# Kernel tuning notes

Measured on AMD Instinct MI355X. Metric: run time of the kernel, lower is better.

## Reference

```python
import jax, jax.numpy as jnp
import numpy as np

B, T, H, S, C = 16, 1024, 1024, 32, 3
NH, DH = 16, 64  # heads, head_dim (NH*DH == H)
GAMMA = 2.0      # focal gamma
EPS = 1e-7       # deberta layer_norm_eps


def setup_inputs() -> dict:
    key = jax.random.key(0)
    ks = jax.random.split(key, 32)
    Hh = H // 2

    def n(k, shape, scale=0.02):
        return jax.random.normal(k, shape, jnp.float32) * scale

    chunk = T // S  # contiguous non-overlapping spans
    heads = jnp.tile(jnp.arange(S, dtype=jnp.int32) * chunk, (B, 1))
    tails = heads + chunk
    inp = {
        'hidden_states': jax.random.normal(ks[0], (B, T, H), jnp.float32),
        'span_head_idxs': heads,
        'span_tail_idxs': tails,
        'span_attention_mask': jnp.ones((B, S), jnp.int32),
        'labels': jax.random.randint(ks[1], (B, S), 0, C, jnp.int32),
        'weights_factor': jax.random.uniform(ks[2], (B, S), jnp.float32) + 0.5,
        # BiLSTM params (torch gate order i,f,g,o)
        'lstm_Wih_f': n(ks[3], (4 * Hh, H)), 'lstm_Whh_f': n(ks[4], (4 * Hh, Hh)), 'lstm_b_f': jnp.zeros((4 * Hh,), jnp.float32),
        'lstm_Wih_b': n(ks[5], (4 * Hh, H)), 'lstm_Whh_b': n(ks[6], (4 * Hh, Hh)), 'lstm_b_b': jnp.zeros((4 * Hh,), jnp.float32),
        # LayerNorm after span pooling
        'ln1_g': jnp.ones((H,), jnp.float32), 'ln1_b': jnp.zeros((H,), jnp.float32),
        # span attention (DebertaV2Attention, relative_attention=False => vanilla MHA)
        'Wq': n(ks[7], (H, H)), 'bq': jnp.zeros((H,), jnp.float32),
        'Wk': n(ks[8], (H, H)), 'bk': jnp.zeros((H,), jnp.float32),
        'Wv': n(ks[9], (H, H)), 'bv': jnp.zeros((H,), jnp.float32),
        'Wo': n(ks[10], (H, H)), 'bo': jnp.zeros((H,), jnp.float32),
        'ln2_g': jnp.ones((H,), jnp.float32), 'ln2_b': jnp.zeros((H,), jnp.float32),
        # classifier
        'Wc': n(ks[11], (H, C)), 'bc': jnp.zeros((C,), jnp.float32),
    }
    return inp


def _layernorm(x, g, b, eps=EPS):
    m = jnp.mean(x, -1, keepdims=True)
    v = jnp.var(x, -1, keepdims=True)
    return (x - m) * jax.lax.rsqrt(v + eps) * g + b


def _lstm_dir(x, Wih, Whh, b, reverse):
    # x: [B,T,H] -> hs [B,T,Hh]
    Hh = Whh.shape[1]
    xs = jnp.einsum('bti,gi->btg', x, Wih) + b  # precompute input projections
    if reverse:
        xs = xs[:, ::-1]

    def step(carry, xt):
        h, c = carry
        g = xt + h @ Whh.T
        i, f, gg, o = jnp.split(g, 4, axis=-1)
        c = jax.nn.sigmoid(f) * c + jax.nn.sigmoid(i) * jnp.tanh(gg)
        h = jax.nn.sigmoid(o) * jnp.tanh(c)
        return (h, c), h

    h0 = jnp.zeros((x.shape[0], Hh), x.dtype)
    _, hs = jax.lax.scan(step, (h0, h0), jnp.swapaxes(xs, 0, 1))
    hs = jnp.swapaxes(hs, 0, 1)
    if reverse:
        hs = hs[:, ::-1]
    return hs


def _forward(hidden_states, span_head_idxs, span_tail_idxs, span_attention_mask,
             labels, weights_factor,
             lstm_Wih_f, lstm_Whh_f, lstm_b_f, lstm_Wih_b, lstm_Whh_b, lstm_b_b,
             ln1_g, ln1_b, Wq, bq, Wk, bk, Wv, bv, Wo, bo, ln2_g, ln2_b, Wc, bc):
    # BiLSTM over tokens
    enc = jnp.concatenate([
        _lstm_dir(hidden_states, lstm_Wih_f, lstm_Whh_f, lstm_b_f, False),
        _lstm_dir(hidden_states, lstm_Wih_b, lstm_Whh_b, lstm_b_b, True),
    ], axis=-1)  # [B,T,H]

    # fused span mean-pooling: mean over tokens p with head < p < tail
    pos = jnp.arange(T)
    smask = (pos[None, None, :] > span_head_idxs[:, :, None]) & \
            (pos[None, None, :] < span_tail_idxs[:, :, None])  # [B,S,T]
    smf = smask.astype(enc.dtype)
    counts = jnp.maximum(smf.sum(-1, keepdims=True), 1.0)
    feat = jnp.einsum('bst,bth->bsh', smf, enc) / counts  # [B,S,H]
    feat = _layernorm(feat, ln1_g, ln1_b)

    # span self-attention (standard MHA + residual LayerNorm)
    def split_heads(x):
        return x.reshape(B, S, NH, DH)
    q = split_heads(feat @ Wq + bq)
    k = split_heads(feat @ Wk + bk)
    v = split_heads(feat @ Wv + bv)
    scores = jnp.einsum('bqhd,bkhd->bhqk', q, k) / np.sqrt(DH).astype(np.float32)
    am = span_attention_mask.astype(jnp.bool_)
    m2 = am[:, None, None, :] & am[:, None, :, None]  # [B,1,S,S]
    scores = jnp.where(m2, scores, jnp.float32(-1e9))
    attn = jax.nn.softmax(scores, axis=-1)
    ctx = jnp.einsum('bhqk,bkhd->bqhd', attn, v).reshape(B, S, H)
    feat2 = _layernorm(ctx @ Wo + bo + feat, ln2_g, ln2_b)

    # classifier (dropouts are identity at eval; the 5-way average collapses)
    logits = feat2 @ Wc + bc  # [B,S,C]

    # losses
    logp = jax.nn.log_softmax(logits, axis=-1)
    lab = labels
    valid = (lab >= 0)
    lp_t = jnp.take_along_axis(logp, jnp.clip(lab, 0)[..., None], axis=-1)[..., 0]
    spanm = span_attention_mask.astype(jnp.float32) * valid.astype(jnp.float32)
    ce = -lp_t * weights_factor
    ce_loss = jnp.sum(ce * spanm) / jnp.maximum(jnp.sum(spanm), 1.0)
    pt = jnp.exp(logp)
    mod = (1.0 - pt) ** GAMMA * logp
    ft = -jnp.take_along_axis(mod, jnp.clip(lab, 0)[..., None], axis=-1)[..., 0]
    vm = valid.astype(jnp.float32)
    focal_loss = jnp.sum(ft * vm) / jnp.maximum(jnp.sum(vm), 1.0)
    return ce_loss + focal_loss


def reference(hidden_states, span_head_idxs, span_tail_idxs, span_attention_mask,
              labels, weights_factor,
              lstm_Wih_f, lstm_Whh_f, lstm_b_f, lstm_Wih_b, lstm_Whh_b, lstm_b_b,
              ln1_g, ln1_b, Wq, bq, Wk, bk, Wv, bv, Wo, bo, ln2_g, ln2_b, Wc, bc):
    return _forward(hidden_states, span_head_idxs, span_tail_idxs, span_attention_mask,
                    labels, weights_factor,
                    lstm_Wih_f, lstm_Whh_f, lstm_b_f, lstm_Wih_b, lstm_Whh_b, lstm_b_b,
                    ln1_g, ln1_b, Wq, bq, Wk, bk, Wv, bv, Wo, bo, ln2_g, ln2_b, Wc, bc)
```

## Files before the change

### kernel.cpp

```cpp
#include <hip/hip_runtime.h>
#include <stdint.h>

typedef __attribute__((ext_vector_type(4))) float    f32x4;
typedef __attribute__((ext_vector_type(8))) short    s16x8;
typedef __attribute__((ext_vector_type(4))) uint32_t u32x4;
typedef __attribute__((ext_vector_type(4))) uint16_t u16x4;
typedef __attribute__((ext_vector_type(8))) uint16_t u16x8;

#define SENT 0xFFFFFFFFu

__device__ __forceinline__ uint16_t f2bf(float f) {
    uint32_t u = __float_as_uint(f);
    u = u + 0x7FFFu + ((u >> 16) & 1u);
    return (uint16_t)(u >> 16);
}
__device__ __forceinline__ float bf2f(uint16_t h) {
    return __uint_as_float(((uint32_t)h) << 16);
}
__device__ __forceinline__ float sigm(float x) {
    return __builtin_amdgcn_rcpf(1.0f + __expf(-x));
}
__device__ __forceinline__ float tanh_f(float x) {
    float e = __expf(2.0f * x);
    return 1.0f - 2.0f * __builtin_amdgcn_rcpf(e + 1.0f);
}

__global__ void kinit(uint32_t* __restrict__ hx) {
    size_t i = ((size_t)blockIdx.x * 256 + threadIdx.x) * 4;
    *(u32x4*)(hx + i) = u32x4{SENT, SENT, SENT, SENT};
}

__global__ void kprep(const float* __restrict__ wihf, const float* __restrict__ wihb,
                      const float* __restrict__ whhf, const float* __restrict__ whhb,
                      const float* __restrict__ bq, const float* __restrict__ bk,
                      const float* __restrict__ bv,
                      uint16_t* __restrict__ wihbf, uint16_t* __restrict__ whhbf,
                      float* __restrict__ biasqkv) {
    size_t i = (size_t)blockIdx.x * 256 + threadIdx.x;
    if (i < 2097152) {
        wihbf[i] = f2bf(wihf[i]);
    } else if (i < 4194304) {
        wihbf[i] = f2bf(wihb[i - 2097152]);
    } else if (i < 5242880) {
        whhbf[i - 4194304] = f2bf(whhf[i - 4194304]);
    } else if (i < 6291456) {
        whhbf[i - 4194304] = f2bf(whhb[i - 5242880]);
    } else if (i < 6294528) {
        size_t k = i - 6291456;
        biasqkv[k] = (k < 1024) ? bq[k] : (k < 2048) ? bk[k - 1024] : bv[k - 2048];
    }
}

__global__ void ktrans(const float* __restrict__ Wq, const float* __restrict__ Wk,
                       const float* __restrict__ Wv, const float* __restrict__ Wo,
                       uint16_t* __restrict__ out) {
    const float* W = (blockIdx.z == 0) ? Wq : (blockIdx.z == 1) ? Wk : (blockIdx.z == 2) ? Wv : Wo;
    __shared__ float t[32][33];
    int x  = blockIdx.x * 32 + threadIdx.x;
    int y0 = blockIdx.y * 32 + threadIdx.y;
#pragma unroll
    for (int i = 0; i < 4; i++)
        t[threadIdx.y + 8 * i][threadIdx.x] = W[(size_t)(y0 + 8 * i) * 1024 + x];
    __syncthreads();
    int ox  = blockIdx.y * 32 + threadIdx.x;
    int oy0 = blockIdx.x * 32 + threadIdx.y;
#pragma unroll
    for (int i = 0; i < 4; i++)
        out[((size_t)blockIdx.z * 1024 + oy0 + 8 * i) * 1024 + ox] = f2bf(t[threadIdx.x][threadIdx.y + 8 * i]);
}

template <int AF32>
__global__ __launch_bounds__(256) void gemm_k(const void* __restrict__ Av,
                                              const uint16_t* __restrict__ B,
                                              const float* __restrict__ bias,
                                              uint16_t* __restrict__ C, int M, int N) {
    __shared__ uint16_t lA[128 * 40];
    __shared__ uint16_t lB[128 * 40];
    const int tid = threadIdx.x;
    const int m0 = blockIdx.y * 128, n0 = blockIdx.x * 128;
    const int srow = tid >> 1, skh = (tid & 1) * 16;
    const int lane = tid & 63, wid = tid >> 6;
    const int wm = wid >> 1, wn = wid & 1;
    const int fn = lane & 15, fq = lane >> 4;
    f32x4 acc[4][4];
#pragma unroll
    for (int a = 0; a < 4; a++)
#pragma unroll
        for (int b = 0; b < 4; b++) acc[a][b] = f32x4{0.f, 0.f, 0.f, 0.f};

    for (int kt = 0; kt < 32; kt++) {
        if (AF32) {
            const float* A = (const float*)Av + (size_t)(m0 + srow) * 1024 + kt * 32 + skh;
#pragma unroll
            for (int i = 0; i < 4; i++) {
                f32x4 t = *(const f32x4*)(A + i * 4);
                u16x4 p;
                p[0] = f2bf(t[0]); p[1] = f2bf(t[1]); p[2] = f2bf(t[2]); p[3] = f2bf(t[3]);
                *(u16x4*)&lA[srow * 40 + skh + i * 4] = p;
            }
        } else {
            const uint16_t* A = (const uint16_t*)Av + (size_t)(m0 + srow) * 1024 + kt * 32 + skh;
            *(u16x8*)&lA[srow * 40 + skh]     = *(const u16x8*)(A);
            *(u16x8*)&lA[srow * 40 + skh + 8] = *(const u16x8*)(A + 8);
        }
        const uint16_t* Bp = B + (size_t)(n0 + srow) * 1024 + kt * 32 + skh;
        *(u16x8*)&lB[srow * 40 + skh]     = *(const u16x8*)(Bp);
        *(u16x8*)&lB[srow * 40 + skh + 8] = *(const u16x8*)(Bp + 8);
        __syncthreads();
        s16x8 af[4], bfv[4];
#pragma unroll
        for (int mt = 0; mt < 4; mt++) af[mt] = *(const s16x8*)&lA[(wm * 64 + mt * 16 + fn) * 40 + fq * 8];
#pragma unroll
        for (int nt = 0; nt < 4; nt++) bfv[nt] = *(const s16x8*)&lB[(wn * 64 + nt * 16 + fn) * 40 + fq * 8];
#pragma unroll
        for (int mt = 0; mt < 4; mt++)
#pragma unroll
            for (int nt = 0; nt < 4; nt++)
                acc[mt][nt] = __builtin_amdgcn_mfma_f32_16x16x32_bf16(af[mt], bfv[nt], acc[mt][nt], 0, 0, 0);
        __syncthreads();
    }
#pragma unroll
    for (int nt = 0; nt < 4; nt++) {
        int col = n0 + wn * 64 + nt * 16 + fn;
        float bvv = bias ? bias[col] : 0.0f;
#pragma unroll
        for (int mt = 0; mt < 4; mt++) {
            int row0 = m0 + wm * 64 + mt * 16 + fq * 4;
#pragma unroll
            for (int i = 0; i < 4; i++)
                C[(size_t)(row0 + i) * N + col] = f2bf(acc[mt][nt][i] + bvv);
        }
    }
}

__global__ __launch_bounds__(256, 1) void krecur(const uint16_t* __restrict__ whhbf,
                                                 const uint16_t* __restrict__ xs,
                                                 uint32_t* __restrict__ hx) {
    const int wg = blockIdx.x;
    const int dir = wg >> 3, g = wg & 7;
    const int tid = threadIdx.x;
    const int w = tid >> 6, lane = tid & 63;
    const int j = g * 4 + w;
    const int n = lane & 15, q = lane >> 4;

    __shared__ uint16_t lh[2][8192];

    s16x8 Bf[4][16];
    {
        const uint16_t* wb = whhbf + (size_t)dir * 2048 * 512;
#pragma unroll
        for (int t4 = 0; t4 < 4; t4++)
#pragma unroll
            for (int s = 0; s < 16; s++)
                Bf[t4][s] = *(const s16x8*)(wb + (size_t)(t4 * 512 + j * 16 + n) * 512 + s * 32 + q * 8);
    }
    float c[4] = {0.f, 0.f, 0.f, 0.f};
    const uint16_t* xsp = xs + (size_t)dir * 16384 * 2048;
    uint32_t* hxp = hx + (size_t)dir * 1024 * 4096;

    uint16_t xv[4][4];
    {
        const int pf = dir ? 1023 : 0;
#pragma unroll
        for (int t4 = 0; t4 < 4; t4++)
#pragma unroll
            for (int i = 0; i < 4; i++)
                xv[t4][i] = xsp[((size_t)(4 * q + i) * 1024 + pf) * 2048 + t4 * 512 + j * 16 + n];
    }

    for (int t = 0; t < 1024; t++) {
        const int p = dir ? (1023 - t) : t;
        const int buf = t & 1;

        f32x4 acc[4];
#pragma unroll
        for (int t4 = 0; t4 < 4; t4++) acc[t4] = f32x4{0.f, 0.f, 0.f, 0.f};

        if (t > 0) {
            const int pp = dir ? (p + 1) : (p - 1);
            const uint32_t* hbase = hxp + ((size_t)pp * 16 + n) * 256 + q * 4;
            u32x4 Ah[4];
            for (;;) {
#pragma unroll
                for (int si = 0; si < 4; si++) {
                    const uint32_t* ap = hbase + (w * 4 + si) * 16;
                    asm volatile("global_load_dwordx4 %0, %1, off sc1"
                                 : "=v"(Ah[si]) : "v"(ap) : "memory");
                }
                asm volatile("s_waitcnt vmcnt(0)" ::: "memory");
                uint32_t mx = 0;
#pragma unroll
                for (int si = 0; si < 4; si++)
#pragma unroll
                    for (int wd = 0; wd < 4; wd++) mx = (Ah[si][wd] > mx) ? Ah[si][wd] : mx;
                if (__ballot(mx == SENT) == 0ull) break;
            }
#pragma unroll
            for (int si = 0; si < 4; si++) {
                int s = w * 4 + si;
                *(u32x4*)&lh[buf][s * 512 + q * 128 + n * 8] = Ah[si];
            }
            __syncthreads();
#pragma unroll
            for (int s = 0; s < 16; s++) {
                s16x8 Af = *(const s16x8*)&lh[buf][s * 512 + q * 128 + n * 8];
#pragma unroll
                for (int t4 = 0; t4 < 4; t4++)
                    acc[t4] = __builtin_amdgcn_mfma_f32_16x16x32_bf16(Af, Bf[t4][s], acc[t4], 0, 0, 0);
            }
        }

        uint16_t xn[4][4];
        if (t < 1023) {
            const int pn = dir ? (p - 1) : (p + 1);
#pragma unroll
            for (int t4 = 0; t4 < 4; t4++)
#pragma unroll
                for (int i = 0; i < 4; i++)
                    xn[t4][i] = xsp[((size_t)(4 * q + i) * 1024 + pn) * 2048 + t4 * 512 + j * 16 + n];
        }

        float g4[4][4];
#pragma unroll
        for (int t4 = 0; t4 < 4; t4++)
#pragma unroll
            for (int i = 0; i < 4; i++)
                g4[t4][i] = acc[t4][i] + bf2f(xv[t4][i]);

#pragma unroll
        for (int i = 0; i < 4; i++) {
            float ig = sigm(g4[0][i]);
            float fg = sigm(g4[1][i]);
            float gg = tanh_f(g4[2][i]);
            float og = sigm(g4[3][i]);
            c[i] = fg * c[i] + ig * gg;
            float hv = og * tanh_f(c[i]);
            uint32_t mine = (uint32_t)f2bf(hv);
            uint32_t part = __shfl_xor(mine, 1);
            if ((n & 1) == 0) {
                uint32_t pack = mine | (part << 16);
                __hip_atomic_store(hxp + ((size_t)p * 16 + 4 * q + i) * 256 + j * 8 + (n >> 1),
                                   pack, __ATOMIC_RELAXED, __HIP_MEMORY_SCOPE_AGENT);
            }
        }

        if (t < 1023) {
#pragma unroll
            for (int t4 = 0; t4 < 4; t4++)
#pragma unroll
                for (int i = 0; i < 4; i++) xv[t4][i] = xn[t4][i];
        }
    }
}

__global__ __launch_bounds__(256) void kpool(const uint32_t* __restrict__ hx,
                                             const int* __restrict__ heads,
                                             const int* __restrict__ tails,
                                             const float* __restrict__ g,
                                             const float* __restrict__ bb,
                                             float* __restrict__ feat,
                                             uint16_t* __restrict__ featb) {
    const int m = blockIdx.x;
    const int b = m >> 5;
    const int tid = threadIdx.x;
    const int h0 = tid * 4;
    const int dir = h0 >> 9, hid = h0 & 511;
    int p0 = heads[m] + 1; if (p0 < 0) p0 = 0;
    int p1 = tails[m];     if (p1 > 1024) p1 = 1024;
    float a0 = 0, a1 = 0, a2 = 0, a3 = 0;
    int cnt = p1 - p0; if (cnt < 1) cnt = 1;
    for (int p = p0; p < p1; p++) {
        const uint32_t* e = hx + (((size_t)dir * 1024 + p) * 16 + b) * 256 + (hid >> 1);
        uint32_t w0 = e[0], w1 = e[1];
        a0 += bf2f((uint16_t)(w0 & 0xffff)); a1 += bf2f((uint16_t)(w0 >> 16));
        a2 += bf2f((uint16_t)(w1 & 0xffff)); a3 += bf2f((uint16_t)(w1 >> 16));
    }
    float inv = 1.0f / (float)cnt;
    float x0 = a0 * inv, x1 = a1 * inv, x2 = a2 * inv, x3 = a3 * inv;
    float ls = x0 + x1 + x2 + x3;
    float lq = x0 * x0 + x1 * x1 + x2 * x2 + x3 * x3;
#pragma unroll
    for (int o = 32; o > 0; o >>= 1) { ls += __shfl_down(ls, o); lq += __shfl_down(lq, o); }
    __shared__ float rs_[4], rq_[4], st_[2];
    const int lane = tid & 63, wid = tid >> 6;
    if (lane == 0) { rs_[wid] = ls; rq_[wid] = lq; }
    __syncthreads();
    if (tid == 0) {
        float S = rs_[0] + rs_[1] + rs_[2] + rs_[3];
        float Q = rq_[0] + rq_[1] + rq_[2] + rq_[3];
        float mean = S * (1.0f / 1024.0f);
        float var = Q * (1.0f / 1024.0f) - mean * mean;
        st_[0] = mean;
        st_[1] = rsqrtf(var + 1e-7f);
    }
    __syncthreads();
    float mean = st_[0], rstd = st_[1];
    size_t ob = (size_t)m * 1024 + h0;
    float y0 = (x0 - mean) * rstd * g[h0 + 0] + bb[h0 + 0];
    float y1 = (x1 - mean) * rstd * g[h0 + 1] + bb[h0 + 1];
    float y2 = (x2 - mean) * rstd * g[h0 + 2] + bb[h0 + 2];
    float y3 = (x3 - mean) * rstd * g[h0 + 3] + bb[h0 + 3];
    feat[ob + 0] = y0; feat[ob + 1] = y1; feat[ob + 2] = y2; feat[ob + 3] = y3;
    featb[ob + 0] = f2bf(y0); featb[ob + 1] = f2bf(y1);
    featb[ob + 2] = f2bf(y2); featb[ob + 3] = f2bf(y3);
}

__global__ __launch_bounds__(64) void kattn(const uint16_t* __restrict__ qkv,
                                            const int* __restrict__ am,
                                            uint16_t* __restrict__ ctxb) {
    const int bb_ = blockIdx.x >> 4, nh = blockIdx.x & 15;
    const int lane = threadIdx.x;
    __shared__ float qs[32][65], ks[32][65], vs[32][65];
    __shared__ float ps[32][33];
    for (int s = 0; s < 32; s++) {
        const uint16_t* base = qkv + (size_t)(bb_ * 32 + s) * 3072 + nh * 64;
        qs[s][lane] = bf2f(base[lane]);
        ks[s][lane] = bf2f(base[1024 + lane]);
        vs[s][lane] = bf2f(base[2048 + lane]);
    }
    __syncthreads();
    const int r = lane >> 1, ch = (lane & 1) * 16;
    const int amr = am[bb_ * 32 + r];
    float sc[16];
#pragma unroll
    for (int c0 = 0; c0 < 16; c0++) {
        int cc = ch + c0;
        float a = 0;
        for (int d = 0; d < 64; d++) a += qs[r][d] * ks[cc][d];
        a *= 0.125f;
        if (!(amr && am[bb_ * 32 + cc])) a = -1e9f;
        sc[c0] = a;
    }
    float mx = sc[0];
#pragma unroll
    for (int c0 = 1; c0 < 16; c0++) mx = fmaxf(mx, sc[c0]);
    mx = fmaxf(mx, __shfl_xor(mx, 1));
    float se = 0;
#pragma unroll
    for (int c0 = 0; c0 < 16; c0++) { sc[c0] = __expf(sc[c0] - mx); se += sc[c0]; }
    se += __shfl_xor(se, 1);
    float inv = __builtin_amdgcn_rcpf(se);
#pragma unroll
    for (int c0 = 0; c0 < 16; c0++) ps[r][ch + c0] = sc[c0] * inv;
    __syncthreads();
    for (int r2 = 0; r2 < 32; r2++) {
        float a = 0;
        for (int cc = 0; cc < 32; cc++) a += ps[r2][cc] * vs[cc][lane];
        ctxb[(size_t)(bb_ * 32 + r2) * 1024 + nh * 64 + lane] = f2bf(a);
    }
}

__global__ __launch_bounds__(256) void kln2(const uint16_t* __restrict__ oproj,
                                            const float* __restrict__ feat,
                                            const float* __restrict__ g,
                                            const float* __restrict__ bb,
                                            float* __restrict__ feat2) {
    const int m = blockIdx.x, tid = threadIdx.x;
    const int h0 = tid * 4;
    size_t base = (size_t)m * 1024 + h0;
    u16x4 ov = *(const u16x4*)(oproj + base);
    float x0 = bf2f(ov[0]) + feat[base + 0];
    float x1 = bf2f(ov[1]) + feat[base + 1];
    float x2 = bf2f(ov[2]) + feat[base + 2];
    float x3 = bf2f(ov[3]) + feat[base + 3];
    float ls = x0 + x1 + x2 + x3;
    float lq = x0 * x0 + x1 * x1 + x2 * x2 + x3 * x3;
#pragma unroll
    for (int o = 32; o > 0; o >>= 1) { ls += __shfl_down(ls, o); lq += __shfl_down(lq, o); }
    __shared__ float rs_[4], rq_[4], st_[2];
    const int lane = tid & 63, wid = tid >> 6;
    if (lane == 0) { rs_[wid] = ls; rq_[wid] = lq; }
    __syncthreads();
    if (tid == 0) {
        float S = rs_[0] + rs_[1] + rs_[2] + rs_[3];
        float Q = rq_[0] + rq_[1] + rq_[2] + rq_[3];
        float mean = S * (1.0f / 1024.0f);
        float var = Q * (1.0f / 1024.0f) - mean * mean;
        st_[0] = mean;
        st_[1] = rsqrtf(var + 1e-7f);
    }
    __syncthreads();
    float mean = st_[0], rstd = st_[1];
    feat2[base + 0] = (x0 - mean) * rstd * g[h0 + 0] + bb[h0 + 0];
    feat2[base + 1] = (x1 - mean) * rstd * g[h0 + 1] + bb[h0 + 1];
    feat2[base + 2] = (x2 - mean) * rstd * g[h0 + 2] + bb[h0 + 2];
    feat2[base + 3] = (x3 - mean) * rstd * g[h0 + 3] + bb[h0 + 3];
}

__global__ __launch_bounds__(64) void kloss(const float* __restrict__ feat2,
                                            const float* __restrict__ Wc,
                                            const float* __restrict__ bc,
                                            const int* __restrict__ labels,
                                            const int* __restrict__ am,
                                            const float* __restrict__ wf,
                                            float* __restrict__ accum) {
    const int m = blockIdx.x, lane = threadIdx.x;
    float l0 = 0, l1 = 0, l2 = 0;
    for (int k = lane; k < 1024; k += 64) {
        float f = feat2[(size_t)m * 1024 + k];
        l0 += f * Wc[k * 3 + 0];
        l1 += f * Wc[k * 3 + 1];
        l2 += f * Wc[k * 3 + 2];
    }
#pragma unroll
    for (int o = 32; o > 0; o >>= 1) {
        l0 += __shfl_down(l0, o);
        l1 += __shfl_down(l1, o);
        l2 += __shfl_down(l2, o);
    }
    if (lane == 0) {
        l0 += bc[0]; l1 += bc[1]; l2 += bc[2];
        float mx = fmaxf(l0, fmaxf(l1, l2));
        float e0 = __expf(l0 - mx), e1 = __expf(l1 - mx), e2 = __expf(l2 - mx);
        float lse = mx + __logf(e0 + e1 + e2);
        float lp[3] = {l0 - lse, l1 - lse, l2 - lse};
        int lab = labels[m];
        float validf = (lab >= 0) ? 1.0f : 0.0f;
        int labc = lab < 0 ? 0 : lab;
        float amv = (am[m] != 0) ? 1.0f : 0.0f;
        float spanm = amv * validf;
        float ce = -lp[labc] * wf[m];
        float pt = __expf(lp[labc]);
        float om = 1.0f - pt;
        float ft = -(om * om * lp[labc]);
        atomicAdd(accum + 0, ce * spanm);
        atomicAdd(accum + 1, spanm);
        atomicAdd(accum + 2, ft * validf);
        atomicAdd(accum + 3, validf);
    }
}

__global__ void kfinal(const float* __restrict__ accum, float* __restrict__ out) {
    out[0] = accum[0] / fmaxf(accum[1], 1.0f) + accum[2] / fmaxf(accum[3], 1.0f);
}

extern "C" void kernel_launch(void* const* d_in, const int* in_sizes, int n_in,
                              void* d_out, int out_size, void* d_ws, size_t ws_size,
                              hipStream_t stream) {
    const float* hs   = (const float*)d_in[0];
    const int* heads  = (const int*)d_in[1];
    const int* tails  = (const int*)d_in[2];
    const int* amask  = (const int*)d_in[3];
    const int* labels = (const int*)d_in[4];
    const float* wfac = (const float*)d_in[5];
    const float* wihf = (const float*)d_in[6];
    const float* whhf = (const float*)d_in[7];
    const float* lbf  = (const float*)d_in[8];
    const float* wihb = (const float*)d_in[9];
    const float* whhb = (const float*)d_in[10];
    const float* lbb  = (const float*)d_in[11];
    const float* ln1g = (const float*)d_in[12];
    const float* ln1b = (const float*)d_in[13];
    const float* Wq   = (const float*)d_in[14];
    const float* bq   = (const float*)d_in[15];
    const float* Wk   = (const float*)d_in[16];
    const float* bk   = (const float*)d_in[17];
    const float* Wv   = (const float*)d_in[18];
    const float* bv   = (const float*)d_in[19];
    const float* Wo   = (const float*)d_in[20];
    const float* bo   = (const float*)d_in[21];
    const float* ln2g = (const float*)d_in[22];
    const float* ln2b = (const float*)d_in[23];
    const float* Wc   = (const float*)d_in[24];
    const float* bc   = (const float*)d_in[25];

    char* ws = (char*)d_ws;
    float* accum    = (float*)(ws + 1024);
    uint16_t* whhbf = (uint16_t*)(ws + 4096);
    uint16_t* wihbf = (uint16_t*)(ws + 4198400);
    uint16_t* wqkvo = (uint16_t*)(ws + 12587008);
    float* biasqkv  = (float*)(ws + 20975616);
    uint16_t* xs    = (uint16_t*)(ws + 20987904);
    uint32_t* hx    = (uint32_t*)(ws + 155205632);
    float* feat     = (float*)(ws + 188760064);
    uint16_t* featb = (uint16_t*)(ws + 190857216);
    uint16_t* qkvb  = (uint16_t*)(ws + 191905792);
    uint16_t* ctxb  = (uint16_t*)(ws + 195051520);
    uint16_t* oprojb= (uint16_t*)(ws + 196100096);
    float* feat2    = (float*)(ws + 197148672);

    hipMemsetAsync(ws, 0, 4096, stream);

    kinit<<<8192, 256, 0, stream>>>(hx);

    kprep<<<24588, 256, 0, stream>>>(wihf, wihb, whhf, whhb, bq, bk, bv, wihbf, whhbf, biasqkv);
    ktrans<<<dim3(32, 32, 4), dim3(32, 8), 0, stream>>>(Wq, Wk, Wv, Wo, wqkvo);

    gemm_k<1><<<dim3(16, 128), 256, 0, stream>>>(hs, wihbf, lbf, xs, 16384, 2048);
    gemm_k<1><<<dim3(16, 128), 256, 0, stream>>>(hs, wihbf + (size_t)2048 * 1024, lbb,
                                                 xs + (size_t)16384 * 2048, 16384, 2048);

    krecur<<<16, 256, 0, stream>>>(whhbf, xs, hx);

    kpool<<<512, 256, 0, stream>>>(hx, heads, tails, ln1g, ln1b, feat, featb);

    gemm_k<0><<<dim3(24, 4), 256, 0, stream>>>(featb, wqkvo, biasqkv, qkvb, 512, 3072);

    kattn<<<256, 64, 0, stream>>>(qkvb, amask, ctxb);

    gemm_k<0><<<dim3(8, 4), 256, 0, stream>>>(ctxb, wqkvo + (size_t)3072 * 1024, bo, oprojb, 512, 1024);

    kln2<<<512, 256, 0, stream>>>(oprojb, feat, ln2g, ln2b, feat2);
    kloss<<<512, 64, 0, stream>>>(feat2, Wc, bc, labels, amask, wfac, accum);
    kfinal<<<1, 1, 0, stream>>>(accum, (float*)d_out);
}
```

Before: 4.195 ms.

## Fuse LSTM input-projection GEMM with recurrence via sentinel-flagged streaming

```diff
diff --git a/kernel.cpp b/kernel.cpp
--- a/kernel.cpp
+++ b/kernel.cpp
@@ -25,9 +25,9 @@
     return 1.0f - 2.0f * __builtin_amdgcn_rcpf(e + 1.0f);
 }
 
-__global__ void kinit(uint32_t* __restrict__ hx) {
+__global__ void kinit(uint32_t* __restrict__ base) {
     size_t i = ((size_t)blockIdx.x * 256 + threadIdx.x) * 4;
-    *(u32x4*)(hx + i) = u32x4{SENT, SENT, SENT, SENT};
+    *(u32x4*)(base + i) = u32x4{SENT, SENT, SENT, SENT};
 }
 
 __global__ void kprep(const float* __restrict__ wihf, const float* __restrict__ wihb,
@@ -69,8 +69,7 @@
         out[((size_t)blockIdx.z * 1024 + oy0 + 8 * i) * 1024 + ox] = f2bf(t[threadIdx.x][threadIdx.y + 8 * i]);
 }
 
-template <int AF32>
-__global__ __launch_bounds__(256) void gemm_k(const void* __restrict__ Av,
+__global__ __launch_bounds__(256) void gemm_k(const uint16_t* __restrict__ A0,
                                               const uint16_t* __restrict__ B,
                                               const float* __restrict__ bias,
                                               uint16_t* __restrict__ C, int M, int N) {
@@ -89,20 +88,9 @@
         for (int b = 0; b < 4; b++) acc[a][b] = f32x4{0.f, 0.f, 0.f, 0.f};
 
     for (int kt = 0; kt < 32; kt++) {
-        if (AF32) {
-            const float* A = (const float*)Av + (size_t)(m0 + srow) * 1024 + kt * 32 + skh;
-#pragma unroll
-            for (int i = 0; i < 4; i++) {
-                f32x4 t = *(const f32x4*)(A + i * 4);
-                u16x4 p;
-                p[0] = f2bf(t[0]); p[1] = f2bf(t[1]); p[2] = f2bf(t[2]); p[3] = f2bf(t[3]);
-                *(u16x4*)&lA[srow * 40 + skh + i * 4] = p;
-            }
-        } else {
-            const uint16_t* A = (const uint16_t*)Av + (size_t)(m0 + srow) * 1024 + kt * 32 + skh;
-            *(u16x8*)&lA[srow * 40 + skh]     = *(const u16x8*)(A);
-            *(u16x8*)&lA[srow * 40 + skh + 8] = *(const u16x8*)(A + 8);
-        }
+        const uint16_t* A = A0 + (size_t)(m0 + srow) * 1024 + kt * 32 + skh;
+        *(u16x8*)&lA[srow * 40 + skh]     = *(const u16x8*)(A);
+        *(u16x8*)&lA[srow * 40 + skh + 8] = *(const u16x8*)(A + 8);
         const uint16_t* Bp = B + (size_t)(n0 + srow) * 1024 + kt * 32 + skh;
         *(u16x8*)&lB[srow * 40 + skh]     = *(const u16x8*)(Bp);
         *(u16x8*)&lB[srow * 40 + skh + 8] = *(const u16x8*)(Bp + 8);
@@ -133,122 +121,240 @@
     }
 }
 
-__global__ __launch_bounds__(256, 1) void krecur(const uint16_t* __restrict__ whhbf,
-                                                 const uint16_t* __restrict__ xs,
+__global__ __launch_bounds__(256, 1) void kfused(const uint16_t* __restrict__ whhbf,
+                                                 const uint16_t* __restrict__ wihbf,
+                                                 const float* __restrict__ hs,
+                                                 const float* __restrict__ lbf,
+                                                 const float* __restrict__ lbb,
+                                                 uint16_t* __restrict__ xs,
                                                  uint32_t* __restrict__ hx) {
-    const int wg = blockIdx.x;
-    const int dir = wg >> 3, g = wg & 7;
-    const int tid = threadIdx.x;
-    const int w = tid >> 6, lane = tid & 63;
-    const int j = g * 4 + w;
-    const int n = lane & 15, q = lane >> 4;
-
-    __shared__ uint16_t lh[2][8192];
-
-    s16x8 Bf[4][16];
-    {
-        const uint16_t* wb = whhbf + (size_t)dir * 2048 * 512;
-#pragma unroll
-        for (int t4 = 0; t4 < 4; t4++)
-#pragma unroll
-            for (int s = 0; s < 16; s++)
-                Bf[t4][s] = *(const s16x8*)(wb + (size_t)(t4 * 512 + j * 16 + n) * 512 + s * 32 + q * 8);
-    }
-    float c[4] = {0.f, 0.f, 0.f, 0.f};
-    const uint16_t* xsp = xs + (size_t)dir * 16384 * 2048;
-    uint32_t* hxp = hx + (size_t)dir * 1024 * 4096;
-
-    uint16_t xv[4][4];
-    {
-        const int pf = dir ? 1023 : 0;
-#pragma unroll
-        for (int t4 = 0; t4 < 4; t4++)
-#pragma unroll
-            for (int i = 0; i < 4; i++)
-                xv[t4][i] = xsp[((size_t)(4 * q + i) * 1024 + pf) * 2048 + t4 * 512 + j * 16 + n];
-    }
-
-    for (int t = 0; t < 1024; t++) {
-        const int p = dir ? (1023 - t) : t;
-        const int buf = t & 1;
-
-        f32x4 acc[4];
-#pragma unroll
-        for (int t4 = 0; t4 < 4; t4++) acc[t4] = f32x4{0.f, 0.f, 0.f, 0.f};
-
-        if (t > 0) {
-            const int pp = dir ? (p + 1) : (p - 1);
-            const uint32_t* hbase = hxp + ((size_t)pp * 16 + n) * 256 + q * 4;
+    __shared__ uint16_t smem[16384];
+
+    if (blockIdx.x < 16) {
+        const int wg = blockIdx.x;
+        const int dir = wg >> 3, g = wg & 7;
+        const int tid = threadIdx.x;
+        const int w = tid >> 6, lane = tid & 63;
+        const int j = g * 4 + w;
+        const int n = lane & 15, q = lane >> 4;
+
+        s16x8 Bf[4][16];
+        {
+            const uint16_t* wb = whhbf + (size_t)dir * 2048 * 512;
+#pragma unroll
+            for (int t4 = 0; t4 < 4; t4++)
+#pragma unroll
+                for (int s = 0; s < 16; s++)
+                    Bf[t4][s] = *(const s16x8*)(wb + (size_t)(t4 * 512 + j * 16 + n) * 512 + s * 32 + q * 8);
+        }
+        float c[4] = {0.f, 0.f, 0.f, 0.f};
+        const uint32_t* xsp32 = (const uint32_t*)(xs + (size_t)dir * 16384 * 2048);
+        uint32_t* hxp = hx + (size_t)dir * 1024 * 4096;
+
+        uint32_t xvA[4][4], xvB[4][4];
+        {
+            const int pf = dir ? 1023 : 0;
+#pragma unroll
+            for (int t4 = 0; t4 < 4; t4++)
+#pragma unroll
+                for (int i = 0; i < 4; i++) {
+                    const uint32_t* ap = xsp32 + ((size_t)(4 * q + i) * 1024 + pf) * 1024
+                                       + ((t4 * 512 + j * 16 + n) >> 1);
+                    asm volatile("global_load_dword %0, %1, off sc1"
+                                 : "=v"(xvA[t4][i]) : "v"(ap) : "memory");
+                }
+        }
+
+        auto rstep = [&](int t, uint32_t (&xc)[4][4], uint32_t (&xn)[4][4]) {
+            const int p = dir ? (1023 - t) : t;
+            const int buf = t & 1;
             u32x4 Ah[4];
-            for (;;) {
+            const uint32_t* hbase = nullptr;
+            if (t > 0) {
+                const int pp = dir ? (p + 1) : (p - 1);
+                hbase = hxp + ((size_t)pp * 16 + n) * 256 + q * 4;
 #pragma unroll
                 for (int si = 0; si < 4; si++) {
                     const uint32_t* ap = hbase + (w * 4 + si) * 16;
                     asm volatile("global_load_dwordx4 %0, %1, off sc1"
                                  : "=v"(Ah[si]) : "v"(ap) : "memory");
                 }
+            }
+            if (t < 1023) {
+                const int pn = dir ? (p - 1) : (p + 1);
+#pragma unroll
+                for (int t4 = 0; t4 < 4; t4++)
+#pragma unroll
+                    for (int i = 0; i < 4; i++) {
+                        const uint32_t* ap = xsp32 + ((size_t)(4 * q + i) * 1024 + pn) * 1024
+                                           + ((t4 * 512 + j * 16 + n) >> 1);
+                        asm volatile("global_load_dword %0, %1, off sc1"
+                                     : "=v"(xn[t4][i]) : "v"(ap) : "memory");
+                    }
+                asm volatile("s_waitcnt vmcnt(16)" ::: "memory");
+            } else {
                 asm volatile("s_waitcnt vmcnt(0)" ::: "memory");
-                uint32_t mx = 0;
-#pragma unroll
-                for (int si = 0; si < 4; si++)
-#pragma unroll
-                    for (int wd = 0; wd < 4; wd++) mx = (Ah[si][wd] > mx) ? Ah[si][wd] : mx;
-                if (__ballot(mx == SENT) == 0ull) break;
             }
-#pragma unroll
-            for (int si = 0; si < 4; si++) {
-                int s = w * 4 + si;
-                *(u32x4*)&lh[buf][s * 512 + q * 128 + n * 8] = Ah[si];
+
+            f32x4 acc[4];
+#pragma unroll
+            for (int t4 = 0; t4 < 4; t4++) acc[t4] = f32x4{0.f, 0.f, 0.f, 0.f};
+
+            if (t > 0) {
+                for (;;) {
+                    uint32_t bad = 0;
+#pragma unroll
+                    for (int si = 0; si < 4; si++)
+#pragma unroll
+                        for (int wd = 0; wd < 4; wd++)
+                            if (Ah[si][wd] == SENT) bad = 1;
+                    if (__ballot(bad) == 0ull) break;
+#pragma unroll
+                    for (int si = 0; si < 4; si++) {
+                        const uint32_t* ap = hbase + (w * 4 + si) * 16;
+                        asm volatile("global_load_dwordx4 %0, %1, off sc1"
+                                     : "=v"(Ah[si]) : "v"(ap) : "memory");
+                    }
+                    asm volatile("s_waitcnt vmcnt(0)" ::: "memory");
+                }
+#pragma unroll
+                for (int si = 0; si < 4; si++) {
+                    int s = w * 4 + si;
+                    *(u32x4*)&smem[buf * 8192 + s * 512 + q * 128 + n * 8] = Ah[si];
+                }
+                __syncthreads();
+#pragma unroll
+                for (int s = 0; s < 16; s++) {
+                    s16x8 Af = *(const s16x8*)&smem[buf * 8192 + s * 512 + q * 128 + n * 8];
+#pragma unroll
+                    for (int t4 = 0; t4 < 4; t4++)
+                        acc[t4] = __builtin_amdgcn_mfma_f32_16x16x32_bf16(Af, Bf[t4][s], acc[t4], 0, 0, 0);
+                }
             }
+
+            for (;;) {
+                uint32_t bad = 0;
+#pragma unroll
+                for (int t4 = 0; t4 < 4; t4++)
+#pragma unroll
+                    for (int i = 0; i < 4; i++)
+                        if (xc[t4][i] == SENT) bad = 1;
+                if (__ballot(bad) == 0ull) break;
+#pragma unroll
+                for (int t4 = 0; t4 < 4; t4++)
+#pragma unroll
+                    for (int i = 0; i < 4; i++) {
+                        const uint32_t* ap = xsp32 + ((size_t)(4 * q + i) * 1024 + p) * 1024
+                                           + ((t4 * 512 + j * 16 + n) >> 1);
+                        asm volatile("global_load_dword %0, %1, off sc1"
+                                     : "=v"(xc[t4][i]) : "v"(ap) : "memory");
+                    }
+                asm volatile("s_waitcnt vmcnt(0)" ::: "memory");
+            }
+
+            float g4[4][4];
+#pragma unroll
+            for (int t4 = 0; t4 < 4; t4++)
+#pragma unroll
+                for (int i = 0; i < 4; i++) {
+                    uint32_t pr = xc[t4][i];
+                    uint16_t xv16 = (n & 1) ? (uint16_t)(pr >> 16) : (uint16_t)(pr & 0xffff);
+                    g4[t4][i] = acc[t4][i] + bf2f(xv16);
+                }
+#pragma unroll
+            for (int i = 0; i < 4; i++) {
+                float ig = sigm(g4[0][i]);
+                float fg = sigm(g4[1][i]);
+                float gg = tanh_f(g4[2][i]);
+                float og = sigm(g4[3][i]);
+                c[i] = fg * c[i] + ig * gg;
+                float hv = og * tanh_f(c[i]);
+                uint32_t mine = (uint32_t)f2bf(hv);
+                uint32_t part = __shfl_xor(mine, 1);
+                if ((n & 1) == 0) {
+                    uint32_t pack = mine | (part << 16);
+                    __hip_atomic_store(hxp + ((size_t)p * 16 + 4 * q + i) * 256 + j * 8 + (n >> 1),
+                                       pack, __ATOMIC_RELAXED, __HIP_MEMORY_SCOPE_AGENT);
+                }
+            }
+        };
+
+        for (int t2 = 0; t2 < 1024; t2 += 2) {
+            rstep(t2,     xvA, xvB);
+            rstep(t2 + 1, xvB, xvA);
+        }
+    } else {
+        const int gb = blockIdx.x - 16;
+        const int dirg = gb & 1;
+        const int k = gb >> 1;
+        const int prorder = k >> 8;
+        const int rem = k & 255;
+        const int bidx = rem >> 4;
+        const int ntile = rem & 15;
+        const int prange = dirg ? (7 - prorder) : prorder;
+        const size_t mbase = (size_t)bidx * 1024 + (size_t)prange * 128;
+        const int n0 = ntile * 128;
+        const uint16_t* Bw = wihbf + (size_t)dirg * 2048 * 1024;
+        const float* biasg = dirg ? lbb : lbf;
+        uint16_t* Cx = xs + (size_t)dirg * 16384 * 2048;
+
+        uint16_t* lA = smem;
+        uint16_t* lB = smem + 5120;
+        const int tid = threadIdx.x;
+        const int srow = tid >> 1, skh = (tid & 1) * 16;
+        const int lane = tid & 63, wid = tid >> 6;
+        const int wm = wid >> 1, wn = wid & 1;
+        const int fn = lane & 15, fq = lane >> 4;
+        f32x4 acc[4][4];
+#pragma unroll
+        for (int a = 0; a < 4; a++)
+#pragma unroll
+            for (int b = 0; b < 4; b++) acc[a][b] = f32x4{0.f, 0.f, 0.f, 0.f};
+
+        for (int kt = 0; kt < 32; kt++) {
+            const float* A = hs + (mbase + srow) * 1024 + kt * 32 + skh;
+#pragma unroll
+            for (int i = 0; i < 4; i++) {
+                f32x4 tv = *(const f32x4*)(A + i * 4);
+                u16x4 pk;
+                pk[0] = f2bf(tv[0]); pk[1] = f2bf(tv[1]); pk[2] = f2bf(tv[2]); pk[3] = f2bf(tv[3]);
+                *(u16x4*)&lA[srow * 40 + skh + i * 4] = pk;
+            }
+            const uint16_t* Bp = Bw + (size_t)(n0 + srow) * 1024 + kt * 32 + skh;
+            *(u16x8*)&lB[srow * 40 + skh]     = *(const u16x8*)(Bp);
+            *(u16x8*)&lB[srow * 40 + skh + 8] = *(const u16x8*)(Bp + 8);
             __syncthreads();
-#pragma unroll
-            for (int s = 0; s < 16; s++) {
-                s16x8 Af = *(const s16x8*)&lh[buf][s * 512 + q * 128 + n * 8];
-#pragma unroll
-                for (int t4 = 0; t4 < 4; t4++)
-                    acc[t4] = __builtin_amdgcn_mfma_f32_16x16x32_bf16(Af, Bf[t4][s], acc[t4], 0, 0, 0);
+            s16x8 af[4], bfv[4];
+#pragma unroll
+            for (int mt = 0; mt < 4; mt++) af[mt] = *(const s16x8*)&lA[(wm * 64 + mt * 16 + fn) * 40 + fq * 8];
+#pragma unroll
+            for (int nt = 0; nt < 4; nt++) bfv[nt] = *(const s16x8*)&lB[(wn * 64 + nt * 16 + fn) * 40 + fq * 8];
+#pragma unroll
+            for (int mt = 0; mt < 4; mt++)
+#pragma unroll
+                for (int nt = 0; nt < 4; nt++)
+                    acc[mt][nt] = __builtin_amdgcn_mfma_f32_16x16x32_bf16(af[mt], bfv[nt], acc[mt][nt], 0, 0, 0);
+            __syncthreads();
+        }
+#pragma unroll
+        for (int nt = 0; nt < 4; nt++) {
+            int col = n0 + wn * 64 + nt * 16 + fn;
+            float bvv = biasg[col];
+#pragma unroll
+            for (int mt = 0; mt < 4; mt++) {
+                int rowoff = wm * 64 + mt * 16 + fq * 4;
+#pragma unroll
+                for (int i = 0; i < 4; i++) {
+                    uint32_t mine = (uint32_t)f2bf(acc[mt][nt][i] + bvv);
+                    uint32_t part = __shfl_xor(mine, 1);
+                    if ((fn & 1) == 0) {
+                        uint32_t pack = mine | (part << 16);
+                        size_t grow = mbase + rowoff + i;
+                        __hip_atomic_store((uint32_t*)(Cx + grow * 2048 + col), pack,
+                                           __ATOMIC_RELAXED, __HIP_MEMORY_SCOPE_AGENT);
+                    }
+                }
             }
-        }
-
-        uint16_t xn[4][4];
-        if (t < 1023) {
-            const int pn = dir ? (p - 1) : (p + 1);
-#pragma unroll
-            for (int t4 = 0; t4 < 4; t4++)
-#pragma unroll
-                for (int i = 0; i < 4; i++)
-                    xn[t4][i] = xsp[((size_t)(4 * q + i) * 1024 + pn) * 2048 + t4 * 512 + j * 16 + n];
-        }
-
-        float g4[4][4];
-#pragma unroll
-        for (int t4 = 0; t4 < 4; t4++)
-#pragma unroll
-            for (int i = 0; i < 4; i++)
-                g4[t4][i] = acc[t4][i] + bf2f(xv[t4][i]);
-
-#pragma unroll
-        for (int i = 0; i < 4; i++) {
-            float ig = sigm(g4[0][i]);
-            float fg = sigm(g4[1][i]);
-            float gg = tanh_f(g4[2][i]);
-            float og = sigm(g4[3][i]);
-            c[i] = fg * c[i] + ig * gg;
-            float hv = og * tanh_f(c[i]);
-            uint32_t mine = (uint32_t)f2bf(hv);
-            uint32_t part = __shfl_xor(mine, 1);
-            if ((n & 1) == 0) {
-                uint32_t pack = mine | (part << 16);
-                __hip_atomic_store(hxp + ((size_t)p * 16 + 4 * q + i) * 256 + j * 8 + (n >> 1),
-                                   pack, __ATOMIC_RELAXED, __HIP_MEMORY_SCOPE_AGENT);
-            }
-        }
-
-        if (t < 1023) {
-#pragma unroll
-            for (int t4 = 0; t4 < 4; t4++)
-#pragma unroll
-                for (int i = 0; i < 4; i++) xv[t4][i] = xn[t4][i];
         }
     }
 }
@@ -481,24 +587,20 @@
 
     hipMemsetAsync(ws, 0, 4096, stream);
 
-    kinit<<<8192, 256, 0, stream>>>(hx);
+    kinit<<<40960, 256, 0, stream>>>((uint32_t*)(ws + 20987904));
 
     kprep<<<24588, 256, 0, stream>>>(wihf, wihb, whhf, whhb, bq, bk, bv, wihbf, whhbf, biasqkv);
     ktrans<<<dim3(32, 32, 4), dim3(32, 8), 0, stream>>>(Wq, Wk, Wv, Wo, wqkvo);
 
-    gemm_k<1><<<dim3(16, 128), 256, 0, stream>>>(hs, wihbf, lbf, xs, 16384, 2048);
-    gemm_k<1><<<dim3(16, 128), 256, 0, stream>>>(hs, wihbf + (size_t)2048 * 1024, lbb,
-                                                 xs + (size_t)16384 * 2048, 16384, 2048);
-
-    krecur<<<16, 256, 0, stream>>>(whhbf, xs, hx);
+    kfused<<<4112, 256, 0, stream>>>(whhbf, wihbf, hs, lbf, lbb, xs, hx);
 
     kpool<<<512, 256, 0, stream>>>(hx, heads, tails, ln1g, ln1b, feat, featb);
 
-    gemm_k<0><<<dim3(24, 4), 256, 0, stream>>>(featb, wqkvo, biasqkv, qkvb, 512, 3072);
+    gemm_k<<<dim3(24, 4), 256, 0, stream>>>(featb, wqkvo, biasqkv, qkvb, 512, 3072);
 
     kattn<<<256, 64, 0, stream>>>(qkvb, amask, ctxb);
 
-    gemm_k<0><<<dim3(8, 4), 256, 0, stream>>>(ctxb, wqkvo + (size_t)3072 * 1024, bo, oprojb, 512, 1024);
+    gemm_k<<<dim3(8, 4), 256, 0, stream>>>(ctxb, wqkvo + (size_t)3072 * 1024, bo, oprojb, 512, 1024);
 
     kln2<<<512, 256, 0, stream>>>(oprojb, feat, ln2g, ln2b, feat2);
     kloss<<<512, 64, 0, stream>>>(feat2, Wc, bc, labels, amask, wfac, accum);
```

Result: faster. 4.101 ms (-2.2%).
